# Performance work log

Measured on AMD Instinct MI355X. Metric: run time of the kernel, lower is better.

Reference implementation:

```python
import jax, jax.numpy as jnp
import numpy as np

NUM_CLASSES = 4
STRENGTH_INTER = 1.0
MOMENTUM = 0.99
EPS = 1e-8
LOG2 = 0.6931471805599453


def setup_inputs() -> dict:
    key = jax.random.key(0)
    k1, k2, k3, k4 = jax.random.split(key, 4)
    B, F, C, D, H, W = 2, 32, NUM_CLASSES, 64, 128, 128
    return {
        "features_to_modulate": jax.random.normal(k1, (B, F, D, H, W), dtype=jnp.float32),
        "logits_A": jax.random.normal(k2, (B, C, D, H, W), dtype=jnp.float32),
        "logits_B": jax.random.normal(k3, (B, C, D, H, W), dtype=jnp.float32),
        "pseudo_labels": jax.random.randint(k4, (B, D, H, W), 0, C, dtype=jnp.int64),
        "global_class_ranks": jnp.arange(C, dtype=jnp.float32),
    }


def _gamma_map(logits_A, logits_B, pseudo_labels, global_class_ranks):
    # JS-divergence disagreement map, summed over class channel (axis=1)
    logpA = jax.nn.log_softmax(logits_A, axis=1)
    logpB = jax.nn.log_softmax(logits_B, axis=1)
    pA = jnp.exp(logpA)
    pB = jnp.exp(logpB)
    logM = jnp.log(0.5 * (pA + pB) + EPS)
    kl_A = jnp.sum(pA * (logpA - logM), axis=1)  # [B,D,H,W]
    kl_B = jnp.sum(pB * (logpB - logM), axis=1)
    dis = 0.5 * (kl_A + kl_B)

    # per-class stats via segment reductions (single pass instead of per-class masking)
    lab_flat = pseudo_labels.reshape(-1)
    dis_flat = dis.reshape(-1)
    counts = jax.ops.segment_sum(jnp.ones_like(dis_flat), lab_flat, num_segments=NUM_CLASSES)
    seg_min = jax.ops.segment_min(dis_flat, lab_flat, num_segments=NUM_CLASSES)
    seg_max = jax.ops.segment_max(dis_flat, lab_flat, num_segments=NUM_CLASSES)
    present = counts > 0
    # EMA buffers start uninitialized (init: min=0, max=log 2); first call copies batch stats
    cls_min = jnp.where(present, seg_min, 0.0)
    cls_max = jnp.where(present, seg_max, LOG2)

    dmin = cls_min[pseudo_labels]
    dmax = cls_max[pseudo_labels]
    norm = jnp.where(dmax > dmin, (dis - dmin) / (dmax - dmin + EPS), 0.5)

    inter_term = 1.0 - global_class_ranks / (NUM_CLASSES - 1)
    inter_map = STRENGTH_INTER * inter_term[pseudo_labels]
    return 1.0 + inter_map * norm  # [B,D,H,W]


def reference(features_to_modulate, logits_A, logits_B, pseudo_labels, global_class_ranks):
    gamma_map = _gamma_map(logits_A, logits_B, pseudo_labels, global_class_ranks)
    scaled = features_to_modulate * gamma_map[:, None]  # broadcast over channel dim
    return scaled, gamma_map
```

## Files before the change

### kernel.cpp

```cpp
#include <hip/hip_runtime.h>
#include <hip/hip_bf16.h>

#define S_VOX  1048576
#define NVOX   2097152
#define NCLS   4
#define NFEAT  32
#define FEAT_ELEMS 67108864
#define EPS_F  1e-8f
#define LOG2_F 0.6931471805599453f
#define DIS_BLOCKS 1024

typedef float f32x4 __attribute__((ext_vector_type(4)));

__device__ __forceinline__ unsigned f2key(float f) {
    unsigned u = __float_as_uint(f);
    return (u & 0x80000000u) ? ~u : (u | 0x80000000u);
}
__device__ __forceinline__ float key2f(unsigned k) {
    unsigned u = (k & 0x80000000u) ? (k & 0x7FFFFFFFu) : ~k;
    return __uint_as_float(u);
}


__global__ void k_prolog(const unsigned* __restrict__ lab32, int* __restrict__ flag) {
    int t = threadIdx.x;
    unsigned even = lab32[2 * t];
    unsigned odd  = lab32[2 * t + 1];
    unsigned long long oddnz  = __ballot(odd  != 0u);
    unsigned long long evennz = __ballot(even != 0u);
    if (t == 0) *flag = (oddnz == 0ull && evennz != 0ull) ? 1 : 0;
}

__global__ void __launch_bounds__(256)
k_dis(const float* __restrict__ lA, const float* __restrict__ lB,
      const unsigned* __restrict__ lab32, const int* __restrict__ i64flag,
      unsigned* __restrict__ disp, unsigned* __restrict__ partials) {
    __shared__ unsigned smin[NCLS], smax[NCLS];
    if (threadIdx.x < NCLS) { smin[threadIdx.x] = 0xFFFFFFFFu; smax[threadIdx.x] = 0u; }
    __syncthreads();

    const int lstride = 1 + *i64flag;
    unsigned lmin[NCLS] = {0xFFFFFFFFu, 0xFFFFFFFFu, 0xFFFFFFFFu, 0xFFFFFFFFu};
    unsigned lmax[NCLS] = {0u, 0u, 0u, 0u};

    const int nquad = NVOX / 4;
    for (int q = blockIdx.x * blockDim.x + threadIdx.x; q < nquad;
         q += gridDim.x * blockDim.x) {
        const int g = q << 2;
        const int b = g >> 20;
        const int v = g & (S_VOX - 1);
        const size_t abase = ((size_t)b * NCLS) * S_VOX + v;

        float4 a0 = *(const float4*)(lA + abase);
        float4 a1 = *(const float4*)(lA + abase + S_VOX);
        float4 a2 = *(const float4*)(lA + abase + 2 * (size_t)S_VOX);
        float4 a3 = *(const float4*)(lA + abase + 3 * (size_t)S_VOX);
        float4 c0 = *(const float4*)(lB + abase);
        float4 c1 = *(const float4*)(lB + abase + S_VOX);
        float4 c2 = *(const float4*)(lB + abase + 2 * (size_t)S_VOX);
        float4 c3 = *(const float4*)(lB + abase + 3 * (size_t)S_VOX);

        float dv[4];
        #pragma unroll
        for (int j = 0; j < 4; ++j) {
            float av[NCLS] = { ((const float*)&a0)[j], ((const float*)&a1)[j],
                               ((const float*)&a2)[j], ((const float*)&a3)[j] };
            float bv[NCLS] = { ((const float*)&c0)[j], ((const float*)&c1)[j],
                               ((const float*)&c2)[j], ((const float*)&c3)[j] };
            float maxA = fmaxf(fmaxf(av[0], av[1]), fmaxf(av[2], av[3]));
            float maxB = fmaxf(fmaxf(bv[0], bv[1]), fmaxf(bv[2], bv[3]));
            float eA[NCLS], eB[NCLS];
            float sA = 0.f, sB = 0.f;
            #pragma unroll
            for (int c = 0; c < NCLS; ++c) {
                eA[c] = __expf(av[c] - maxA); sA += eA[c];
                eB[c] = __expf(bv[c] - maxB); sB += eB[c];
            }
            float lseA = __logf(sA), lseB = __logf(sB);
            float rsA = 1.f / sA, rsB = 1.f / sB;
            float kl = 0.f;
            #pragma unroll
            for (int c = 0; c < NCLS; ++c) {
                float pA  = eA[c] * rsA;
                float pB  = eB[c] * rsB;
                float la  = av[c] - maxA - lseA;
                float lb  = bv[c] - maxB - lseB;
                float lM  = __logf(0.5f * (pA + pB) + EPS_F);
                kl += pA * (la - lM) + pB * (lb - lM);
            }
            dv[j] = 0.5f * kl;
        }

        unsigned lbls[4];
        #pragma unroll
        for (int j = 0; j < 4; ++j)
            lbls[j] = lab32[(size_t)(g + j) * lstride] & 3u;

        unsigned pw[4];
        #pragma unroll
        for (int j = 0; j < 4; ++j)
            pw[j] = (__float_as_uint(dv[j]) & ~3u) | lbls[j];
        *(uint4*)(disp + g) = make_uint4(pw[0], pw[1], pw[2], pw[3]);

        #pragma unroll
        for (int j = 0; j < 4; ++j) {
            unsigned key = f2key(dv[j]);
            #pragma unroll
            for (int c = 0; c < NCLS; ++c) {
                if (lbls[j] == (unsigned)c) {
                    lmin[c] = min(lmin[c], key);
                    lmax[c] = max(lmax[c], key);
                }
            }
        }
    }

    #pragma unroll
    for (int off = 32; off > 0; off >>= 1) {
        #pragma unroll
        for (int c = 0; c < NCLS; ++c) {
            unsigned om = (unsigned)__shfl_xor((int)lmin[c], off);
            unsigned oM = (unsigned)__shfl_xor((int)lmax[c], off);
            lmin[c] = min(lmin[c], om);
            lmax[c] = max(lmax[c], oM);
        }
    }
    if ((threadIdx.x & 63) == 0) {
        #pragma unroll
        for (int c = 0; c < NCLS; ++c) {
            atomicMin(&smin[c], lmin[c]);
            atomicMax(&smax[c], lmax[c]);
        }
    }
    __syncthreads();
    if (threadIdx.x < 8) {
        unsigned val = (threadIdx.x < NCLS) ? smin[threadIdx.x] : smax[threadIdx.x - NCLS];
        partials[(size_t)blockIdx.x * 8 + threadIdx.x] = val;
    }
}

__global__ void __launch_bounds__(256)
k_stats(const unsigned* __restrict__ partials, const float* __restrict__ ranks,
        float* __restrict__ params) {
    __shared__ unsigned red[4][8];
    const int tid = threadIdx.x;

    unsigned mn[NCLS] = {0xFFFFFFFFu, 0xFFFFFFFFu, 0xFFFFFFFFu, 0xFFFFFFFFu};
    unsigned mx[NCLS] = {0u, 0u, 0u, 0u};
    #pragma unroll
    for (int s = 0; s < 4; ++s) {
        const unsigned* p = partials + ((size_t)tid * 4 + s) * 8;
        uint4 pmin = *(const uint4*)(p);
        uint4 pmax = *(const uint4*)(p + 4);
        mn[0] = min(mn[0], pmin.x); mn[1] = min(mn[1], pmin.y);
        mn[2] = min(mn[2], pmin.z); mn[3] = min(mn[3], pmin.w);
        mx[0] = max(mx[0], pmax.x); mx[1] = max(mx[1], pmax.y);
        mx[2] = max(mx[2], pmax.z); mx[3] = max(mx[3], pmax.w);
    }
    #pragma unroll
    for (int off = 32; off > 0; off >>= 1) {
        #pragma unroll
        for (int c = 0; c < NCLS; ++c) {
            unsigned om = (unsigned)__shfl_xor((int)mn[c], off);
            unsigned oM = (unsigned)__shfl_xor((int)mx[c], off);
            mn[c] = min(mn[c], om);
            mx[c] = max(mx[c], oM);
        }
    }
    if ((tid & 63) == 0) {
        const int w = tid >> 6;
        #pragma unroll
        for (int c = 0; c < NCLS; ++c) { red[w][c] = mn[c]; red[w][NCLS + c] = mx[c]; }
    }
    __syncthreads();
    if (tid < NCLS) {
        const int c = tid;
        unsigned kmin = 0xFFFFFFFFu, kmax = 0u;
        #pragma unroll
        for (int w = 0; w < 4; ++w) {
            kmin = min(kmin, red[w][c]);
            kmax = max(kmax, red[w][NCLS + c]);
        }
        bool present = (kmin != 0xFFFFFFFFu);
        float dmin = present ? key2f(kmin) : 0.0f;
        float dmax = present ? key2f(kmax) : LOG2_F;
        float inter = 1.0f - ranks[c] * (1.0f / (NCLS - 1));
        float base, mult;
        if (dmax > dmin) {
            float inv = 1.0f / (dmax - dmin + EPS_F);
            mult = inter * inv;
            base = 1.0f - mult * dmin;
        } else {
            mult = 0.0f;
            base = 1.0f + 0.5f * inter;
        }
        params[c] = base;
        params[NCLS + c] = mult;
    }
}

__global__ void __launch_bounds__(256)
k_scale(const float* __restrict__ feat, const unsigned* __restrict__ disp,
        const float* __restrict__ params, float* __restrict__ gamma_out,
        float* __restrict__ out) {
    const float b0 = params[0], b1 = params[1], b2 = params[2], b3 = params[3];
    const float m0 = params[4], m1 = params[5], m2 = params[6], m3 = params[7];

    const size_t nchunk = FEAT_ELEMS / 4096;
    for (size_t cb = blockIdx.x; cb < nchunk; cb += gridDim.x) {
        const int f0 = (int)((cb >> 8) & 31);
        const size_t e0 = (cb << 12) + ((size_t)threadIdx.x << 2);
        const size_t gb = ((cb >> 13) << 20) + ((cb << 12) & (size_t)(S_VOX - 1))
                          + ((size_t)threadIdx.x << 2);

        f32x4 x0 = __builtin_nontemporal_load((const f32x4*)(feat + e0));
        f32x4 x1 = __builtin_nontemporal_load((const f32x4*)(feat + e0 + 1024));
        f32x4 x2 = __builtin_nontemporal_load((const f32x4*)(feat + e0 + 2048));
        f32x4 x3 = __builtin_nontemporal_load((const f32x4*)(feat + e0 + 3072));

        f32x4 ga[4];
        #pragma unroll
        for (int u = 0; u < 4; ++u) {
            uint4 dp = *(const uint4*)(disp + gb + (size_t)u * 1024);
            const unsigned dw[4] = { dp.x, dp.y, dp.z, dp.w };
            #pragma unroll
            for (int j = 0; j < 4; ++j) {
                const unsigned lbl = dw[j] & 3u;
                const float d = __uint_as_float(dw[j]);
                const float bb = (lbl & 1u) ? ((lbl & 2u) ? b3 : b1)
                                            : ((lbl & 2u) ? b2 : b0);
                const float mm = (lbl & 1u) ? ((lbl & 2u) ? m3 : m1)
                                            : ((lbl & 2u) ? m2 : m0);
                ga[u][j] = fmaf(mm, d, bb);
            }
        }

        __builtin_nontemporal_store(x0 * ga[0], (f32x4*)(out + e0));
        __builtin_nontemporal_store(x1 * ga[1], (f32x4*)(out + e0 + 1024));
        __builtin_nontemporal_store(x2 * ga[2], (f32x4*)(out + e0 + 2048));
        __builtin_nontemporal_store(x3 * ga[3], (f32x4*)(out + e0 + 3072));

        if (f0 == 0) {
            #pragma unroll
            for (int u = 0; u < 4; ++u)
                *(f32x4*)(gamma_out + gb + (size_t)u * 1024) = ga[u];
        }
    }
}

extern "C" void kernel_launch(void* const* d_in, const int* in_sizes, int n_in,
                              void* d_out, int out_size, void* d_ws, size_t ws_size,
                              hipStream_t stream) {
    const float*    feat  = (const float*)d_in[0];
    const float*    lA    = (const float*)d_in[1];
    const float*    lB    = (const float*)d_in[2];
    const unsigned* lab32 = (const unsigned*)d_in[3];
    const float*    ranks = (const float*)d_in[4];
    float* out = (float*)d_out;

    char* ws = (char*)d_ws;
    int*      flag     = (int*)(ws + 32);
    float*    params   = (float*)(ws + 64);
    unsigned* disp     = (unsigned*)(ws + 256);
    unsigned* partials = (unsigned*)(ws + 256 + (size_t)NVOX * 4);

    float* gamma_out = out + (size_t)FEAT_ELEMS;

    k_prolog<<<1, 64, 0, stream>>>(lab32, flag);
    k_dis<<<DIS_BLOCKS, 256, 0, stream>>>(lA, lB, lab32, flag, disp, partials);
    k_stats<<<1, 256, 0, stream>>>(partials, ranks, params);
    k_scale<<<8192, 256, 0, stream>>>(feat, disp, params, gamma_out, out);
}
```

Baseline: 124.6 us.

## Fold label-width probe into k_dis, vectorize label loads, double dis grid

Removes the separate single-block prolog launch by having every k_dis block detect the int64-vs-int32 label layout itself through a wavefront ballot into shared memory. Label reads become 128-bit vector loads split by stride instead of four scalar strided loads. The dis grid doubles to 2048 blocks, and k_stats now reduces 8 partials per thread to match. This trades one launch for redundant 128-label probes in every block, plus a slightly larger final reduction.

```diff
diff --git a/kernel.cpp b/kernel.cpp
--- a/kernel.cpp
+++ b/kernel.cpp
@@ -8,7 +8,7 @@
 #define FEAT_ELEMS 67108864
 #define EPS_F  1e-8f
 #define LOG2_F 0.6931471805599453f
-#define DIS_BLOCKS 1024
+#define DIS_BLOCKS 2048
 
 typedef float f32x4 __attribute__((ext_vector_type(4)));
 
@@ -22,24 +22,24 @@
 }
 
 
-__global__ void k_prolog(const unsigned* __restrict__ lab32, int* __restrict__ flag) {
-    int t = threadIdx.x;
-    unsigned even = lab32[2 * t];
-    unsigned odd  = lab32[2 * t + 1];
-    unsigned long long oddnz  = __ballot(odd  != 0u);
-    unsigned long long evennz = __ballot(even != 0u);
-    if (t == 0) *flag = (oddnz == 0ull && evennz != 0ull) ? 1 : 0;
-}
-
 __global__ void __launch_bounds__(256)
 k_dis(const float* __restrict__ lA, const float* __restrict__ lB,
-      const unsigned* __restrict__ lab32, const int* __restrict__ i64flag,
+      const unsigned* __restrict__ lab32,
       unsigned* __restrict__ disp, unsigned* __restrict__ partials) {
     __shared__ unsigned smin[NCLS], smax[NCLS];
+    __shared__ int s_lstride;
     if (threadIdx.x < NCLS) { smin[threadIdx.x] = 0xFFFFFFFFu; smax[threadIdx.x] = 0u; }
+    if (threadIdx.x < 64) {
+        unsigned even = lab32[2 * threadIdx.x];
+        unsigned odd  = lab32[2 * threadIdx.x + 1];
+        unsigned long long oddnz  = __ballot(odd  != 0u);
+        unsigned long long evennz = __ballot(even != 0u);
+        if (threadIdx.x == 0)
+            s_lstride = (oddnz == 0ull && evennz != 0ull) ? 2 : 1;
+    }
     __syncthreads();
 
-    const int lstride = 1 + *i64flag;
+    const int lstride = s_lstride;
     unsigned lmin[NCLS] = {0xFFFFFFFFu, 0xFFFFFFFFu, 0xFFFFFFFFu, 0xFFFFFFFFu};
     unsigned lmax[NCLS] = {0u, 0u, 0u, 0u};
 
@@ -92,9 +92,16 @@
         }
 
         unsigned lbls[4];
-        #pragma unroll
-        for (int j = 0; j < 4; ++j)
-            lbls[j] = lab32[(size_t)(g + j) * lstride] & 3u;
+        if (lstride == 2) {
+            uint4 L0 = *(const uint4*)(lab32 + 2 * (size_t)g);
+            uint4 L1 = *(const uint4*)(lab32 + 2 * (size_t)g + 4);
+            lbls[0] = L0.x & 3u; lbls[1] = L0.z & 3u;
+            lbls[2] = L1.x & 3u; lbls[3] = L1.z & 3u;
+        } else {
+            uint4 L = *(const uint4*)(lab32 + (size_t)g);
+            lbls[0] = L.x & 3u; lbls[1] = L.y & 3u;
+            lbls[2] = L.z & 3u; lbls[3] = L.w & 3u;
+        }
 
         unsigned pw[4];
         #pragma unroll
@@ -148,8 +155,8 @@
     unsigned mn[NCLS] = {0xFFFFFFFFu, 0xFFFFFFFFu, 0xFFFFFFFFu, 0xFFFFFFFFu};
     unsigned mx[NCLS] = {0u, 0u, 0u, 0u};
     #pragma unroll
-    for (int s = 0; s < 4; ++s) {
-        const unsigned* p = partials + ((size_t)tid * 4 + s) * 8;
+    for (int s = 0; s < 8; ++s) {
+        const unsigned* p = partials + ((size_t)tid * 8 + s) * 8;
         uint4 pmin = *(const uint4*)(p);
         uint4 pmax = *(const uint4*)(p + 4);
         mn[0] = min(mn[0], pmin.x); mn[1] = min(mn[1], pmin.y);
@@ -259,15 +266,13 @@
     float* out = (float*)d_out;
 
     char* ws = (char*)d_ws;
-    int*      flag     = (int*)(ws + 32);
     float*    params   = (float*)(ws + 64);
     unsigned* disp     = (unsigned*)(ws + 256);
     unsigned* partials = (unsigned*)(ws + 256 + (size_t)NVOX * 4);
 
     float* gamma_out = out + (size_t)FEAT_ELEMS;
 
-    k_prolog<<<1, 64, 0, stream>>>(lab32, flag);
-    k_dis<<<DIS_BLOCKS, 256, 0, stream>>>(lA, lB, lab32, flag, disp, partials);
+    k_dis<<<DIS_BLOCKS, 256, 0, stream>>>(lA, lB, lab32, disp, partials);
     k_stats<<<1, 256, 0, stream>>>(partials, ranks, params);
     k_scale<<<8192, 256, 0, stream>>>(feat, disp, params, gamma_out, out);
 }
```

After: 120.0 us. 3.6% less time.
